# Kernel optimization log

Hardware: AMD Instinct MI355X
Metric: run time of the kernel (lower is better)

Reference implementation:

```python
import jax, jax.numpy as jnp
import numpy as np

N, F_IN, H, C, K, NLAYER, RWS = 50000, 256, 128, 64, 4, 2, 16
ALPHA = 0.1


def setup_inputs() -> dict:
    key = jax.random.key(0)
    ks = jax.random.split(key, 8)
    x = jax.random.normal(ks[0], (N, F_IN), dtype=jnp.float32)
    ends = jax.random.randint(ks[1], (NLAYER, K, N * RWS), 0, N, dtype=jnp.int32)
    lin0_w = jax.random.normal(ks[2], (H, F_IN), dtype=jnp.float32) * 0.05
    lin0_b = jnp.zeros((H,), jnp.float32)
    lin1_w = jax.random.normal(ks[3], (H, H), dtype=jnp.float32) * 0.05
    lin1_b = jnp.zeros((H,), jnp.float32)
    lout_w = jax.random.normal(ks[4], (C, H), dtype=jnp.float32) * 0.05
    lout_b = jnp.zeros((C,), jnp.float32)
    attl_w = jax.random.normal(ks[5], (NLAYER, H), dtype=jnp.float32) * 0.05
    attl_b = jnp.zeros((NLAYER,), jnp.float32)
    attr_w = jax.random.normal(ks[6], (NLAYER, H), dtype=jnp.float32) * 0.05
    attr_b = jnp.zeros((NLAYER,), jnp.float32)
    # att init per source: alpha*(1-alpha)**k for k=0..K, last entry (1-alpha)**K
    t = ALPHA * (1.0 - ALPHA) ** np.arange(0, K + 1)
    t[-1] = (1.0 - ALPHA) ** K
    att = jnp.asarray(np.tile(t[None, :], (NLAYER, 1)), dtype=jnp.float32)
    return dict(x=x, ends=ends, lin0_w=lin0_w, lin0_b=lin0_b, lin1_w=lin1_w,
                lin1_b=lin1_b, lout_w=lout_w, lout_b=lout_b, attl_w=attl_w,
                attl_b=attl_b, attr_w=attr_w, attr_b=attr_b, att=att)


def _samp_aggr_layer(x, lw, lb, alw, alb, arw, arb, mask, ends_l):
    # x: [N, din] -> h: [N, H]
    h = x @ lw.T + lb
    al = h @ alw + alb  # [N]
    ar = h @ arw + arb  # [N]
    n = h.shape[0]
    agg = mask[0] * h
    for k in range(ends_l.shape[0]):  # K hops (small fixed loop)
        e = ends_l[k]  # [N*rws] walk endpoints
        logits = jax.nn.leaky_relu(al[:, None] + ar[e].reshape(n, RWS), 0.2)
        w = jax.nn.softmax(logits, axis=1)  # per-node softmax over rws samples
        agg = agg + mask[k + 1] * jnp.mean(
            w[:, :, None] * h[e].reshape(n, RWS, -1), axis=1)
    return agg


def reference(x, ends, lin0_w, lin0_b, lin1_w, lin1_b, lout_w, lout_b,
              attl_w, attl_b, attr_w, attr_b, att):
    lws = [(lin0_w, lin0_b), (lin1_w, lin1_b)]
    h = x
    for l in range(NLAYER):
        lw, lb = lws[l]
        h = _samp_aggr_layer(h, lw, lb, attl_w[l], attl_b[l],
                             attr_w[l], attr_b[l], att[l], ends[l])
    out = h @ lout_w.T + lout_b
    return jax.nn.log_softmax(out, axis=1)
```

## Files before the change

kernel.cpp:

```cpp
#include <hip/hip_runtime.h>

#define NN   50000
#define FIN  256
#define HD   128
#define CC   64
#define KK   4
#define RWSS 16
#define NRW  (NN*RWSS)
#define KNRW (KK*NRW)

typedef unsigned int   uint32;
typedef unsigned short ushort_t;

typedef __attribute__((ext_vector_type(8))) short short8v;
typedef __attribute__((ext_vector_type(4))) float float4v;
typedef __attribute__((ext_vector_type(4))) uint32 uint4v;
typedef __attribute__((ext_vector_type(2))) float float2v;

static __device__ __forceinline__ float bf16lo(uint32 u) {
    return __uint_as_float(u << 16);
}
static __device__ __forceinline__ float bf16hi(uint32 u) {
    return __uint_as_float(u & 0xFFFF0000u);
}
static __device__ __forceinline__ ushort_t f2bf16(float f) {
    uint32 u = __float_as_uint(f);
    uint32 r = u + 0x7FFFu + ((u >> 16) & 1u);
    return (ushort_t)(r >> 16);
}

#if __has_builtin(__builtin_amdgcn_cvt_pk_fp8_f32) && __has_builtin(__builtin_amdgcn_cvt_pk_f32_fp8)
#define FP8_HW 1
#define WGT_SCALE 1.0f
static __device__ __forceinline__ uint32 enc_e4m3(float f) {
    return (uint32)__builtin_amdgcn_cvt_pk_fp8_f32(f, f, 0, false) & 0xFFu;
}
#else
#define FP8_HW 0
#define WGT_SCALE 0x1p120f
static __device__ __forceinline__ uint32 enc_e4m3(float f) {
    const uint32 u    = __float_as_uint(f);
    const uint32 sign = (u >> 24) & 0x80u;
    const uint32 au   = u & 0x7FFFFFFFu;
    const uint32 r    = au + 0x7FFFFu + ((au >> 20) & 1u);
    int v = (int)(r >> 20) - 960;
    v = v < 0 ? 0 : (v > 127 ? 127 : v);
    return sign | (uint32)v;
}
#endif

static __device__ __forceinline__ void pk_fma_fp8x4(
    uint32 d, float2v w2, float2v* acc2)
{
#if FP8_HW
    const float2v lo = __builtin_amdgcn_cvt_pk_f32_fp8(d, false);
    const float2v hi = __builtin_amdgcn_cvt_pk_f32_fp8(d, true);
    acc2[0] = __builtin_elementwise_fma(lo, w2, acc2[0]);
    acc2[1] = __builtin_elementwise_fma(hi, w2, acc2[1]);
#else
    float2v lo, hi;
    {
        const uint32 b0 = d & 0xFFu, b1 = (d >> 8) & 0xFFu;
        const uint32 b2 = (d >> 16) & 0xFFu, b3 = (d >> 24) & 0xFFu;
        lo.x = __uint_as_float(((b0 & 0x80u) << 24) | ((b0 & 0x7Fu) << 20));
        lo.y = __uint_as_float(((b1 & 0x80u) << 24) | ((b1 & 0x7Fu) << 20));
        hi.x = __uint_as_float(((b2 & 0x80u) << 24) | ((b2 & 0x7Fu) << 20));
        hi.y = __uint_as_float(((b3 & 0x80u) << 24) | ((b3 & 0x7Fu) << 20));
    }
    acc2[0] = __builtin_elementwise_fma(lo, w2, acc2[0]);
    acc2[1] = __builtin_elementwise_fma(hi, w2, acc2[1]);
#endif
}

static __device__ __forceinline__ uint4 packw(const float* p) {
    const float4 w0 = *(const float4*)p;
    const float4 w1 = *(const float4*)(p + 4);
    uint4 q;
    q.x = (uint32)f2bf16(w0.x) | ((uint32)f2bf16(w0.y) << 16);
    q.y = (uint32)f2bf16(w0.z) | ((uint32)f2bf16(w0.w) << 16);
    q.z = (uint32)f2bf16(w1.x) | ((uint32)f2bf16(w1.y) << 16);
    q.w = (uint32)f2bf16(w1.z) | ((uint32)f2bf16(w1.w) << 16);
    return q;
}

__global__ __launch_bounds__(256) void prep_w_kernel(
    const float* __restrict__ w0, const float* __restrict__ w1,
    const float* __restrict__ wo,
    uint4* __restrict__ t0, uint4* __restrict__ t1, uint4* __restrict__ to_)
{
    const int idx = blockIdx.x * 256 + threadIdx.x;
    if (idx < 4096) {
        const int jj = idx & 127, k8 = idx >> 7;
        t0[idx] = packw(w0 + (size_t)jj * FIN + 8 * k8);
    } else if (idx < 6144) {
        const int li = idx - 4096;
        const int jj = li & 127, k8 = li >> 7;
        t1[li] = packw(w1 + (size_t)jj * HD + 8 * k8);
    } else if (idx < 7168) {
        const int li = idx - 6144;
        const int jj = li & 63, k8 = li >> 6;
        to_[li] = packw(wo + (size_t)jj * HD + 8 * k8);
    }
}

template<int DIN, bool ABF16>
__global__ __launch_bounds__(256) void linear_mfma_kernel(
    const void* __restrict__ Ain, const uint4* __restrict__ W16,
    const float* __restrict__ bias,
    const float* __restrict__ alw, const float* __restrict__ alb,
    const float* __restrict__ arw, const float* __restrict__ arb,
    unsigned char* __restrict__ h8s, float* __restrict__ al, float* __restrict__ ar)
{
    const int tid  = threadIdx.x;
    const int wid  = tid >> 6;
    const int lane = tid & 63;
    const int mrow = lane & 15;
    const int kq   = lane >> 4;
    const int row  = blockIdx.x * 64 + wid * 16 + mrow;
    const int arow = row < NN ? row : NN - 1;

    float4v acc[8];
#pragma unroll
    for (int t = 0; t < 8; ++t) acc[t] = (float4v){0.f, 0.f, 0.f, 0.f};

    for (int f0 = 0; f0 < DIN; f0 += 32) {
        short8v a;
        if constexpr (ABF16) {
            a = *(const short8v*)((const ushort_t*)Ain + (size_t)arow * DIN + f0 + 8 * kq);
        } else {
            const float* ap = (const float*)Ain + (size_t)arow * DIN + f0 + 8 * kq;
            const float4 a0 = *(const float4*)ap;
            const float4 a1 = *(const float4*)(ap + 4);
            a[0] = (short)f2bf16(a0.x); a[1] = (short)f2bf16(a0.y);
            a[2] = (short)f2bf16(a0.z); a[3] = (short)f2bf16(a0.w);
            a[4] = (short)f2bf16(a1.x); a[5] = (short)f2bf16(a1.y);
            a[6] = (short)f2bf16(a1.z); a[7] = (short)f2bf16(a1.w);
        }
        const int k8 = (f0 >> 3) + kq;
#pragma unroll
        for (int t = 0; t < 8; ++t) {
            const short8v b = ((const short8v*)W16)[(k8 << 7) + 16 * t + mrow];
            acc[t] = __builtin_amdgcn_mfma_f32_16x16x32_bf16(a, b, acc[t], 0, 0, 0);
        }
    }

    float pa[4] = {0.f, 0.f, 0.f, 0.f};
    float pr[4] = {0.f, 0.f, 0.f, 0.f};
    float hb[8][4];
#pragma unroll
    for (int t = 0; t < 8; ++t) {
        const float bj = bias[16 * t + mrow];
        const float wl = alw[16 * t + mrow];
        const float wr = arw[16 * t + mrow];
#pragma unroll
        for (int g = 0; g < 4; ++g) {
            const float h = acc[t][g] + bj;
            hb[t][g] = h;
            pa[g] = fmaf(h, wl, pa[g]);
            pr[g] = fmaf(h, wr, pr[g]);
        }
    }
    const int rbase = blockIdx.x * 64 + wid * 16 + 4 * kq;
#pragma unroll
    for (int g = 0; g < 4; ++g) {
        const int orow = rbase + g;
        if (orow < NN) {
#pragma unroll
            for (int t = 0; t < 8; ++t) {
                h8s[(size_t)(t >> 2) * (NN * 64) + (size_t)orow * 64 +
                    16 * (t & 3) + mrow] = (unsigned char)enc_e4m3(hb[t][g]);
            }
        }
    }
#pragma unroll
    for (int o = 8; o >= 1; o >>= 1) {
#pragma unroll
        for (int g = 0; g < 4; ++g) {
            pa[g] += __shfl_xor(pa[g], o, 16);
            pr[g] += __shfl_xor(pr[g], o, 16);
        }
    }
    if (mrow == 0) {
#pragma unroll
        for (int g = 0; g < 4; ++g) {
            const int orow = rbase + g;
            if (orow < NN) {
                al[orow] = pa[g] + alb[0];
                ar[orow] = pr[g] + arb[0];
            }
        }
    }
}

__global__ __launch_bounds__(256) void prep_pairs_kernel(
    const int* __restrict__ ends_l, const float* __restrict__ al,
    const float* __restrict__ ar, const float* __restrict__ att_l,
    uint32* __restrict__ pw)
{
    const int wv   = threadIdx.x >> 6;
    const int lane = threadIdx.x & 63;
    const int node = blockIdx.x * 4 + wv;
    const int k    = lane >> 4;
    const int j    = lane & 15;

    const int e = __builtin_nontemporal_load(ends_l + (size_t)k * NRW + node * RWSS + j);
    float lg = al[node] + ar[e];
    lg = (lg > 0.f) ? lg : 0.2f * lg;
    float m = lg;
#pragma unroll
    for (int o = 8; o >= 1; o >>= 1) m = fmaxf(m, __shfl_xor(m, o, 16));
    const float ex = __expf(lg - m);
    float s = ex;
#pragma unroll
    for (int o = 8; o >= 1; o >>= 1) s += __shfl_xor(s, o, 16);
    const float w = ex / s * att_l[k + 1] * (1.0f / RWSS);
    const uint32 packed = ((uint32)f2bf16(w) << 16) | (uint32)e;
    __builtin_nontemporal_store(packed, pw + (size_t)node * 64 + lane);
}

__global__ __launch_bounds__(256, 4) void aggr_slice_kernel(
    const unsigned char* __restrict__ h8s, const uint32* __restrict__ pw,
    const float* __restrict__ att_l, ushort_t* __restrict__ agg16)
{
    const int bid = blockIdx.x;
    const int xcd = bid & 7;
    const int s   = xcd >> 2;
    const int ng  = (bid >> 3) + (xcd & 3) * 782;
    if (ng >= 3125) return;
    const int node0 = ng * 16;

    __shared__ uint32 pair_s[16 * 68];
    const int tid = threadIdx.x;
    {
        const uint4v p4 = __builtin_nontemporal_load(
            (const uint4v*)(pw + (size_t)node0 * 64) + tid);
        const int nl = tid >> 4;
        const int sm = (4 * tid) & 63;
        *(uint4v*)&pair_s[nl * 68 + sm] = p4;
    }
    __syncthreads();

    const int lane = tid & 63;
    const int w    = tid >> 6;
    const int g    = lane >> 4;
    const int r    = (lane >> 2) & 3;
    const int q    = lane & 3;
    const int nl   = w * 4 + g;
    const uint32 qb = (uint32)(q << 4);
    const unsigned char* hbase = h8s + (size_t)s * (NN * 64);
    const uint32* ps = &pair_s[nl * 68 + r];

    float2v acc2[8];
#pragma unroll
    for (int c = 0; c < 8; ++c) acc2[c] = (float2v){0.f, 0.f};

    uint32 pr16[16];
    uint4v vv[16];
#pragma unroll
    for (int i = 0; i < 16; ++i) {
        pr16[i] = ps[4 * i];
        vv[i]   = *(const uint4v*)(hbase + (((pr16[i] & 0xFFFFu) << 6) + qb));
    }
    __builtin_amdgcn_sched_barrier(0);
#pragma unroll
    for (int i = 0; i < 16; ++i) {
        const float wf = __uint_as_float(pr16[i] & 0xFFFF0000u) * WGT_SCALE;
        const float2v w2 = {wf, wf};
        pk_fma_fp8x4(vv[i].x, w2, acc2 + 0);
        pk_fma_fp8x4(vv[i].y, w2, acc2 + 2);
        pk_fma_fp8x4(vv[i].z, w2, acc2 + 4);
        pk_fma_fp8x4(vv[i].w, w2, acc2 + 6);
    }

#pragma unroll
    for (int c = 0; c < 8; ++c) {
        acc2[c].x += __shfl_xor(acc2[c].x, 4, 16);
        acc2[c].y += __shfl_xor(acc2[c].y, 4, 16);
        acc2[c].x += __shfl_xor(acc2[c].x, 8, 16);
        acc2[c].y += __shfl_xor(acc2[c].y, 8, 16);
    }

    if (r == 0) {
        const int node = node0 + nl;
        const uint4v v = *(const uint4v*)(hbase + (((uint32)node << 6) + qb));
        const float a0 = att_l[0] * WGT_SCALE;
        const float2v a2 = {a0, a0};
        pk_fma_fp8x4(v.x, a2, acc2 + 0);
        pk_fma_fp8x4(v.y, a2, acc2 + 2);
        pk_fma_fp8x4(v.z, a2, acc2 + 4);
        pk_fma_fp8x4(v.w, a2, acc2 + 6);
        uint4v o1, o2;
        o1.x = (uint32)f2bf16(acc2[0].x) | ((uint32)f2bf16(acc2[0].y) << 16);
        o1.y = (uint32)f2bf16(acc2[1].x) | ((uint32)f2bf16(acc2[1].y) << 16);
        o1.z = (uint32)f2bf16(acc2[2].x) | ((uint32)f2bf16(acc2[2].y) << 16);
        o1.w = (uint32)f2bf16(acc2[3].x) | ((uint32)f2bf16(acc2[3].y) << 16);
        o2.x = (uint32)f2bf16(acc2[4].x) | ((uint32)f2bf16(acc2[4].y) << 16);
        o2.y = (uint32)f2bf16(acc2[5].x) | ((uint32)f2bf16(acc2[5].y) << 16);
        o2.z = (uint32)f2bf16(acc2[6].x) | ((uint32)f2bf16(acc2[6].y) << 16);
        o2.w = (uint32)f2bf16(acc2[7].x) | ((uint32)f2bf16(acc2[7].y) << 16);
        char* dst = (char*)agg16 + (size_t)node * 256 + s * 128 + q * 32;
        __builtin_nontemporal_store(o1, (uint4v*)dst);
        __builtin_nontemporal_store(o2, (uint4v*)(dst + 16));
    }
}

__global__ __launch_bounds__(256) void out_mfma_kernel(
    const ushort_t* __restrict__ agg16, const uint4* __restrict__ WO16,
    const float* __restrict__ lb, float* __restrict__ outp)
{
    const int tid  = threadIdx.x;
    const int wid  = tid >> 6;
    const int lane = tid & 63;
    const int mrow = lane & 15;
    const int kq   = lane >> 4;
    const int row  = blockIdx.x * 64 + wid * 16 + mrow;
    const int arow = row < NN ? row : NN - 1;

    float4v acc[4];
#pragma unroll
    for (int t = 0; t < 4; ++t) acc[t] = (float4v){0.f, 0.f, 0.f, 0.f};

#pragma unroll
    for (int f0 = 0; f0 < HD; f0 += 32) {
        const short8v a = *(const short8v*)(agg16 + (size_t)arow * HD + f0 + 8 * kq);
        const int k8 = (f0 >> 3) + kq;
#pragma unroll
        for (int t = 0; t < 4; ++t) {
            const short8v b = ((const short8v*)WO16)[(k8 << 6) + 16 * t + mrow];
            acc[t] = __builtin_amdgcn_mfma_f32_16x16x32_bf16(a, b, acc[t], 0, 0, 0);
        }
    }

    float v[4][4];
    float mx[4] = {-1e30f, -1e30f, -1e30f, -1e30f};
#pragma unroll
    for (int t = 0; t < 4; ++t) {
        const float bj = lb[16 * t + mrow];
#pragma unroll
        for (int g = 0; g < 4; ++g) {
            v[t][g] = acc[t][g] + bj;
            mx[g] = fmaxf(mx[g], v[t][g]);
        }
    }
#pragma unroll
    for (int o = 8; o >= 1; o >>= 1)
#pragma unroll
        for (int g = 0; g < 4; ++g) mx[g] = fmaxf(mx[g], __shfl_xor(mx[g], o, 16));
    float sm[4] = {0.f, 0.f, 0.f, 0.f};
#pragma unroll
    for (int t = 0; t < 4; ++t)
#pragma unroll
        for (int g = 0; g < 4; ++g) sm[g] += __expf(v[t][g] - mx[g]);
#pragma unroll
    for (int o = 8; o >= 1; o >>= 1)
#pragma unroll
        for (int g = 0; g < 4; ++g) sm[g] += __shfl_xor(sm[g], o, 16);
    float lgs[4];
#pragma unroll
    for (int g = 0; g < 4; ++g) lgs[g] = __logf(sm[g]);

    const int rbase = blockIdx.x * 64 + wid * 16 + 4 * kq;
#pragma unroll
    for (int g = 0; g < 4; ++g) {
        const int orow = rbase + g;
        if (orow < NN) {
#pragma unroll
            for (int t = 0; t < 4; ++t)
                outp[(size_t)orow * CC + 16 * t + mrow] = v[t][g] - mx[g] - lgs[g];
        }
    }
}

extern "C" void kernel_launch(void* const* d_in, const int* in_sizes, int n_in,
                              void* d_out, int out_size, void* d_ws, size_t ws_size,
                              hipStream_t stream)
{
    const float* x      = (const float*)d_in[0];
    const int*   ends   = (const int*)  d_in[1];
    const float* lin0_w = (const float*)d_in[2];
    const float* lin0_b = (const float*)d_in[3];
    const float* lin1_w = (const float*)d_in[4];
    const float* lin1_b = (const float*)d_in[5];
    const float* lout_w = (const float*)d_in[6];
    const float* lout_b = (const float*)d_in[7];
    const float* attl_w = (const float*)d_in[8];
    const float* attl_b = (const float*)d_in[9];
    const float* attr_w = (const float*)d_in[10];
    const float* attr_b = (const float*)d_in[11];
    const float* att    = (const float*)d_in[12];
    float* outp = (float*)d_out;

    unsigned char* h8s   = (unsigned char*)d_ws;
    ushort_t*      agg16 = (ushort_t*)(h8s + (size_t)2 * NN * 64);
    float*         albuf = (float*)(agg16 + (size_t)NN * HD);
    float*         arbuf = albuf + NN;
    uint32*        pw    = (uint32*)(arbuf + NN);
    uint4*         t0    = (uint4*)(pw + (size_t)KNRW);
    uint4*         t1    = t0 + 4096;
    uint4*         to_   = t1 + 2048;

    const int lin_grid  = (NN + 63) / 64;
    const int nb4       = NN / 4;
    const int aggr_grid = 8 * 782;

    prep_w_kernel<<<28, 256, 0, stream>>>(lin0_w, lin1_w, lout_w, t0, t1, to_);

    linear_mfma_kernel<FIN, false><<<lin_grid, 256, 0, stream>>>(
        x, t0, lin0_b, attl_w, attl_b, attr_w, attr_b, h8s, albuf, arbuf);
    prep_pairs_kernel<<<nb4, 256, 0, stream>>>(ends, albuf, arbuf, att, pw);
    aggr_slice_kernel<<<aggr_grid, 256, 0, stream>>>(h8s, pw, att, agg16);

    linear_mfma_kernel<HD, true><<<lin_grid, 256, 0, stream>>>(
        agg16, t1, lin1_b, attl_w + HD, attl_b + 1, attr_w + HD, attr_b + 1,
        h8s, albuf, arbuf);
    prep_pairs_kernel<<<nb4, 256, 0, stream>>>(ends + KNRW, albuf, arbuf,
                                               att + (KK + 1), pw);
    aggr_slice_kernel<<<aggr_grid, 256, 0, stream>>>(h8s, pw, att + (KK + 1), agg16);

    out_mfma_kernel<<<lin_grid, 256, 0, stream>>>(agg16, to_, lout_b, outp);
}
```

Baseline: 161.7 us.

## Stage bf16 attention-right scores in LDS for walk-weight softmax gather

Stores the per-node right attention score as bf16 and has each prep_pairs block copy the whole array into shared memory, then process 64 nodes per block with random gathers served from LDS. The intent is to replace scattered global gathers with LDS lookups and to halve the ar buffer size. It costs a large LDS footprint that limits occupancy and a full array reload per block, and it reduces logit precision. The output kernel also switches to nontemporal loads and stores.

Result: slower. 307.2 us (+90.0%).

```diff
diff --git a/kernel.cpp b/kernel.cpp
--- a/kernel.cpp
+++ b/kernel.cpp
@@ -109,7 +109,8 @@
     const float* __restrict__ bias,
     const float* __restrict__ alw, const float* __restrict__ alb,
     const float* __restrict__ arw, const float* __restrict__ arb,
-    unsigned char* __restrict__ h8s, float* __restrict__ al, float* __restrict__ ar)
+    unsigned char* __restrict__ h8s, float* __restrict__ al,
+    ushort_t* __restrict__ ar16)
 {
     const int tid  = threadIdx.x;
     const int wid  = tid >> 6;
@@ -185,8 +186,8 @@
         for (int g = 0; g < 4; ++g) {
             const int orow = rbase + g;
             if (orow < NN) {
-                al[orow] = pa[g] + alb[0];
-                ar[orow] = pr[g] + arb[0];
+                al[orow]   = pa[g] + alb[0];
+                ar16[orow] = f2bf16(pr[g] + arb[0]);
             }
         }
     }
@@ -194,28 +195,44 @@
 
 __global__ __launch_bounds__(256) void prep_pairs_kernel(
     const int* __restrict__ ends_l, const float* __restrict__ al,
-    const float* __restrict__ ar, const float* __restrict__ att_l,
+    const ushort_t* __restrict__ ar16, const float* __restrict__ att_l,
     uint32* __restrict__ pw)
 {
-    const int wv   = threadIdx.x >> 6;
-    const int lane = threadIdx.x & 63;
-    const int node = blockIdx.x * 4 + wv;
+    __shared__ uint4v ar_s4[NN / 8];
+    const int tid = threadIdx.x;
+    for (int i = tid; i < NN / 8; i += 256) {
+        ar_s4[i] = __builtin_nontemporal_load((const uint4v*)ar16 + i);
+    }
+    __syncthreads();
+    const ushort_t* ar_s = (const ushort_t*)ar_s4;
+
+    const int wv   = tid >> 6;
+    const int lane = tid & 63;
     const int k    = lane >> 4;
     const int j    = lane & 15;
-
-    const int e = __builtin_nontemporal_load(ends_l + (size_t)k * NRW + node * RWSS + j);
-    float lg = al[node] + ar[e];
-    lg = (lg > 0.f) ? lg : 0.2f * lg;
-    float m = lg;
-#pragma unroll
-    for (int o = 8; o >= 1; o >>= 1) m = fmaxf(m, __shfl_xor(m, o, 16));
-    const float ex = __expf(lg - m);
-    float s = ex;
-#pragma unroll
-    for (int o = 8; o >= 1; o >>= 1) s += __shfl_xor(s, o, 16);
-    const float w = ex / s * att_l[k + 1] * (1.0f / RWSS);
-    const uint32 packed = ((uint32)f2bf16(w) << 16) | (uint32)e;
-    __builtin_nontemporal_store(packed, pw + (size_t)node * 64 + lane);
+    const float attk = att_l[k + 1] * (1.0f / RWSS);
+
+#pragma unroll 4
+    for (int p = 0; p < 16; ++p) {
+        const int node = blockIdx.x * 64 + p * 4 + wv;
+        if (node < NN) {
+            const int e = __builtin_nontemporal_load(
+                ends_l + (size_t)k * NRW + node * RWSS + j);
+            const float are = __uint_as_float((uint32)ar_s[e] << 16);
+            float lg = al[node] + are;
+            lg = (lg > 0.f) ? lg : 0.2f * lg;
+            float m = lg;
+#pragma unroll
+            for (int o = 8; o >= 1; o >>= 1) m = fmaxf(m, __shfl_xor(m, o, 16));
+            const float ex = __expf(lg - m);
+            float s = ex;
+#pragma unroll
+            for (int o = 8; o >= 1; o >>= 1) s += __shfl_xor(s, o, 16);
+            const float w = ex / s * attk;
+            const uint32 packed = ((uint32)f2bf16(w) << 16) | (uint32)e;
+            __builtin_nontemporal_store(packed, pw + (size_t)node * 64 + lane);
+        }
+    }
 }
 
 __global__ __launch_bounds__(256, 4) void aggr_slice_kernel(
@@ -322,7 +339,8 @@
 
 #pragma unroll
     for (int f0 = 0; f0 < HD; f0 += 32) {
-        const short8v a = *(const short8v*)(agg16 + (size_t)arow * HD + f0 + 8 * kq);
+        const short8v a = __builtin_nontemporal_load(
+            (const short8v*)(agg16 + (size_t)arow * HD + f0 + 8 * kq));
         const int k8 = (f0 >> 3) + kq;
 #pragma unroll
         for (int t = 0; t < 4; ++t) {
@@ -366,7 +384,9 @@
         if (orow < NN) {
 #pragma unroll
             for (int t = 0; t < 4; ++t)
-                outp[(size_t)orow * CC + 16 * t + mrow] = v[t][g] - mx[g] - lgs[g];
+                __builtin_nontemporal_store(
+                    v[t][g] - mx[g] - lgs[g],
+                    outp + (size_t)orow * CC + 16 * t + mrow);
         }
     }
 }
@@ -393,28 +413,28 @@
     unsigned char* h8s   = (unsigned char*)d_ws;
     ushort_t*      agg16 = (ushort_t*)(h8s + (size_t)2 * NN * 64);
     float*         albuf = (float*)(agg16 + (size_t)NN * HD);
-    float*         arbuf = albuf + NN;
-    uint32*        pw    = (uint32*)(arbuf + NN);
+    ushort_t*      ar16  = (ushort_t*)(albuf + NN);
+    uint32*        pw    = (uint32*)(ar16 + NN);
     uint4*         t0    = (uint4*)(pw + (size_t)KNRW);
     uint4*         t1    = t0 + 4096;
     uint4*         to_   = t1 + 2048;
 
     const int lin_grid  = (NN + 63) / 64;
-    const int nb4       = NN / 4;
+    const int pp_grid   = (NN + 63) / 64;
     const int aggr_grid = 8 * 782;
 
     prep_w_kernel<<<28, 256, 0, stream>>>(lin0_w, lin1_w, lout_w, t0, t1, to_);
 
     linear_mfma_kernel<FIN, false><<<lin_grid, 256, 0, stream>>>(
-        x, t0, lin0_b, attl_w, attl_b, attr_w, attr_b, h8s, albuf, arbuf);
-    prep_pairs_kernel<<<nb4, 256, 0, stream>>>(ends, albuf, arbuf, att, pw);
+        x, t0, lin0_b, attl_w, attl_b, attr_w, attr_b, h8s, albuf, ar16);
+    prep_pairs_kernel<<<pp_grid, 256, 0, stream>>>(ends, albuf, ar16, att, pw);
     aggr_slice_kernel<<<aggr_grid, 256, 0, stream>>>(h8s, pw, att, agg16);
 
     linear_mfma_kernel<HD, true><<<lin_grid, 256, 0, stream>>>(
         agg16, t1, lin1_b, attl_w + HD, attl_b + 1, attr_w + HD, attr_b + 1,
-        h8s, albuf, arbuf);
-    prep_pairs_kernel<<<nb4, 256, 0, stream>>>(ends + KNRW, albuf, arbuf,
-                                               att + (KK + 1), pw);
+        h8s, albuf, ar16);
+    prep_pairs_kernel<<<pp_grid, 256, 0, stream>>>(ends + KNRW, albuf, ar16,
+                                                   att + (KK + 1), pw);
     aggr_slice_kernel<<<aggr_grid, 256, 0, stream>>>(h8s, pw, att + (KK + 1), agg16);
 
     out_mfma_kernel<<<lin_grid, 256, 0, stream>>>(agg16, to_, lout_b, outp);
```
